# Optimization experiments

Measured on AMD Instinct MI355X. Metric: run time of the kernel, lower is better.

## Reference

```python
import jax, jax.numpy as jnp
import numpy as np
from jax import lax

EPS = 1e-12  # F.normalize eps


def setup_inputs() -> dict:
    key = jax.random.key(0)
    k1, k2, k3, k4 = jax.random.split(key, 4)
    B, C, H, W = 4, 192, 256, 256
    h = 4
    x = jax.random.normal(k1, (B, C, H, W), dtype=jnp.float32)
    qkv_w = jax.random.normal(k2, (3 * C, C), dtype=jnp.float32) * (1.0 / np.sqrt(C))
    dw_w = jax.random.normal(k3, (3 * C, 1, 3, 3), dtype=jnp.float32) * (1.0 / 3.0)
    temp = jnp.ones((h, 1, 1), dtype=jnp.float32)
    proj_w = jax.random.normal(k4, (C, C), dtype=jnp.float32) * (1.0 / np.sqrt(C))
    return {"x": x, "qkv_w": qkv_w, "dw_w": dw_w, "temp": temp, "proj_w": proj_w}


def _l2norm_lastdim(t):
    # F.normalize(t, dim=-1): divide by max(||t||_2, eps)
    n = jnp.sqrt(jnp.sum(t * t, axis=-1, keepdims=True))
    return t / jnp.maximum(n, EPS)


def reference(x, qkv_w, dw_w, temp, proj_w):
    B, C, H, W = x.shape
    h = temp.shape[0]
    D = C // h
    # 1x1 conv (qkv): [B,C,H,W] x [3C,C] -> [B,3C,H,W]
    qkv = jnp.einsum('bchw,oc->bohw', x, qkv_w)
    # depthwise 3x3 conv, padding=1, groups=3C
    qkv = lax.conv_general_dilated(
        qkv, dw_w, window_strides=(1, 1), padding='SAME',
        feature_group_count=3 * C,
        dimension_numbers=('NCHW', 'OIHW', 'NCHW'))
    q, k, v = jnp.split(qkv, 3, axis=1)
    # [B, h, D, HW]
    q = q.reshape(B, h, D, H * W)
    k = k.reshape(B, h, D, H * W)
    v = v.reshape(B, h, D, H * W)
    q = _l2norm_lastdim(q)
    k = _l2norm_lastdim(k)
    # channel attention: [B,h,D,D]
    attn = jnp.einsum('bhdn,bhen->bhde', q, k) * temp[None]
    attn = jax.nn.softmax(attn, axis=-1)
    out = jnp.einsum('bhde,bhen->bhdn', attn, v).reshape(B, C, H, W)
    # 1x1 proj
    return jnp.einsum('bchw,oc->bohw', out, proj_w)
```

## Files before the change

kernel.cpp:

```cpp
#include <hip/hip_runtime.h>

typedef unsigned int uint;
typedef unsigned short ushort;
typedef __attribute__((ext_vector_type(8))) short bf16x8;
typedef __attribute__((ext_vector_type(4))) float f32x4;

#define HWSZ 65536
#define CIN 192
#define C3 576
#define CQK 384

typedef __attribute__((address_space(1))) const void gvoid_c;
typedef __attribute__((address_space(3))) void lvoid;

__device__ __forceinline__ void async16(void* l, const void* g) {
  __builtin_amdgcn_global_load_lds((gvoid_c*)g, (lvoid*)l, 16, 0, 0);
}

__device__ __forceinline__ ushort f2bf(float f) {
  uint u = __float_as_uint(f);
  return (ushort)((u + 0x7fffu + ((u >> 16) & 1u)) >> 16);
}
__device__ __forceinline__ float bflo(uint u) { return __uint_as_float(u << 16); }
__device__ __forceinline__ float bfhi(uint u) { return __uint_as_float(u & 0xffff0000u); }

__global__ __launch_bounds__(256) void k0_transpose(const float* __restrict__ x,
                                                    ushort* __restrict__ xT) {
  __shared__ ushort lds_t[192 * 66];
  int id = blockIdx.x;
  int n0 = (id & 1023) << 6;
  int b = id >> 10;
  int tid = threadIdx.x;
  int nl = tid & 63;
  int cq = tid >> 6;
  const float* xb = x + (long)b * CIN * HWSZ + n0;
#pragma unroll 4
  for (int j = 0; j < 48; ++j) {
    int c = cq + 4 * j;
    lds_t[c * 66 + nl] = f2bf(xb[(long)c * HWSZ + nl]);
  }
  __syncthreads();
  ushort* ob = xT + (long)b * HWSZ * CIN + (long)n0 * CIN;
  int l = tid & 63, w = tid >> 6;
#pragma unroll
  for (int jj = 0; jj < 6; ++jj) {
    int n = w * 16 + (l & 15);
    int m = jj * 4 + (l >> 4);
    int cb = m * 8;
    ushort v[8];
#pragma unroll
    for (int k = 0; k < 8; ++k) v[k] = lds_t[(cb + k) * 66 + n];
    uint4 pk;
    pk.x = (uint)v[0] | ((uint)v[1] << 16);
    pk.y = (uint)v[2] | ((uint)v[3] << 16);
    pk.z = (uint)v[4] | ((uint)v[5] << 16);
    pk.w = (uint)v[6] | ((uint)v[7] << 16);
    *(uint4*)(ob + (long)n * CIN + cb) = pk;
  }
}

__global__ __launch_bounds__(256) void k0_cvtw(const float* __restrict__ w,
                                               ushort* __restrict__ wb, int nelem) {
  int i = (blockIdx.x * 256 + threadIdx.x) * 4;
  if (i + 3 < nelem) {
    float4 f = *(const float4*)(w + i);
    ushort4 o;
    o.x = f2bf(f.x); o.y = f2bf(f.y); o.z = f2bf(f.z); o.w = f2bf(f.w);
    *(ushort4*)(wb + i) = o;
  }
}

template <typename TOut>
__global__ __launch_bounds__(512, 6) void gemm_nt(const ushort* __restrict__ A, long a_bstride,
                                                  const ushort* __restrict__ B, long b_bstride,
                                                  TOut* __restrict__ D, long d_bstride,
                                                  int mtiles) {
  __shared__ ushort lds[23040];
  int idx = blockIdx.x;
  int ntile = idx & 511;
  int bm = idx >> 9;
  int mtile = bm % mtiles;
  int b = bm / mtiles;
  int tid = threadIdx.x;
  int lane = tid & 63;
  int wv = tid >> 6;
  int wm = wv >> 1, wn = wv & 1;
  int lanelo = lane & 15, laneq = lane >> 4;

  const ushort* Ab = A + a_bstride * b + (long)mtile * 192 * 192;
  const ushort* Bb = B + b_bstride * b + (long)ntile * 128 * 192;

  f32x4 acc[3][4] = {};

  for (int kit = 0; kit < 3; ++kit) {
#pragma unroll
    for (int i = 0; i < 6; ++i) {
      int wbase = i * 512 + wv * 64;
      if (wbase < 2880) {
        int c = wbase + lane;
        bool isA = c < 1728;
        int local = isA ? c : c - 1728;
        int row = local / 9;
        int sub = local % 9;
        if (sub < 8) {
          const ushort* g = (isA ? Ab : Bb) + row * 192 + kit * 64 + sub * 8;
          async16((char*)lds + wbase * 16, g);
        }
      }
    }
    __syncthreads();
#pragma unroll
    for (int ks = 0; ks < 2; ++ks) {
      bf16x8 af[3], bf[4];
#pragma unroll
      for (int mt = 0; mt < 3; ++mt) {
        int m = wm * 48 + mt * 16 + lanelo;
        af[mt] = *(const bf16x8*)((const char*)lds + m * 144 + ks * 64 + laneq * 16);
      }
#pragma unroll
      for (int nt = 0; nt < 4; ++nt) {
        int n = wn * 64 + nt * 16 + lanelo;
        bf[nt] = *(const bf16x8*)((const char*)lds + 27648 + n * 144 + ks * 64 + laneq * 16);
      }
#pragma unroll
      for (int mt = 0; mt < 3; ++mt)
#pragma unroll
        for (int nt = 0; nt < 4; ++nt)
          acc[mt][nt] = __builtin_amdgcn_mfma_f32_16x16x32_bf16(af[mt], bf[nt], acc[mt][nt], 0, 0, 0);
    }
    __syncthreads();
  }

  TOut* Db = D + d_bstride * b;
  int colb = ntile * 128 + wn * 64 + lanelo;
#pragma unroll
  for (int mt = 0; mt < 3; ++mt)
#pragma unroll
    for (int nt = 0; nt < 4; ++nt)
#pragma unroll
      for (int r = 0; r < 4; ++r) {
        long row = (long)(mtile * 192 + wm * 48 + mt * 16 + laneq * 4 + r);
        float v = acc[mt][nt][r];
        if constexpr (sizeof(TOut) == 2)
          Db[row * HWSZ + colb + nt * 16] = f2bf(v);
        else
          Db[row * HWSZ + colb + nt * 16] = v;
      }
}

template <typename TOut>
__global__ __launch_bounds__(512, 4) void gemm_nn(const ushort* __restrict__ A, long a_bstride,
                                                  const ushort* __restrict__ B, long b_bstride,
                                                  TOut* __restrict__ D, long d_bstride,
                                                  int mtiles) {
  __shared__ ushort lds[18432];
  int idx = blockIdx.x;
  int ntile = idx & 1023;
  int bm = idx >> 10;
  int mtile = bm % mtiles;
  int b = bm / mtiles;
  int tid = threadIdx.x;
  int lane = tid & 63;
  int wv = tid >> 6;
  int wm = wv >> 1, wn = wv & 1;
  int lanelo = lane & 15, laneq = lane >> 4;

  const ushort* Ab = A + a_bstride * b + (long)mtile * 192 * 192;
  const ushort* Bb = B + b_bstride * b + (long)ntile * 64;

  int cs = tid >> 3, chk = tid & 7;
  ushort* lb = lds + 13824;

  f32x4 acc[3][2] = {};

  for (int kit = 0; kit < 3; ++kit) {
    uint4 bv = *(const uint4*)(Bb + (long)(kit * 64 + cs) * HWSZ + chk * 8);
#pragma unroll
    for (int i = 0; i < 4; ++i) {
      int wbase = i * 512 + wv * 64;
      if (wbase < 1728) {
        int cc = wbase + lane;
        int row = cc / 9, sub = cc % 9;
        if (sub < 8) {
          const ushort* g = Ab + row * 192 + kit * 64 + sub * 8;
          async16((char*)lds + wbase * 16, g);
        }
      }
    }
    union { uint4 q; ushort u[8]; } pk;
    pk.q = bv;
    int colbase = (((cs >> 3) ^ chk) << 3) | (cs & 7);
#pragma unroll
    for (int j = 0; j < 8; ++j)
      lb[(chk * 8 + j) * 72 + colbase] = pk.u[j];
    __syncthreads();
#pragma unroll
    for (int ks = 0; ks < 2; ++ks) {
      bf16x8 af[3], bf[2];
#pragma unroll
      for (int mt = 0; mt < 3; ++mt) {
        int m = wm * 48 + mt * 16 + lanelo;
        af[mt] = *(const bf16x8*)((const char*)lds + m * 144 + ks * 64 + laneq * 16);
      }
#pragma unroll
      for (int nt = 0; nt < 2; ++nt) {
        int n = wn * 32 + nt * 16 + lanelo;
        int cb = ks * 4 + laneq;
        bf[nt] = *(const bf16x8*)((const char*)lds + 27648 + n * 144 +
                                  ((cb ^ ((n >> 3) & 7)) << 4));
      }
#pragma unroll
      for (int mt = 0; mt < 3; ++mt)
#pragma unroll
        for (int nt = 0; nt < 2; ++nt)
          acc[mt][nt] = __builtin_amdgcn_mfma_f32_16x16x32_bf16(af[mt], bf[nt], acc[mt][nt], 0, 0, 0);
    }
    __syncthreads();
  }

  TOut* Db = D + d_bstride * b;
  int colb = ntile * 64 + wn * 32 + lanelo;
#pragma unroll
  for (int mt = 0; mt < 3; ++mt)
#pragma unroll
    for (int nt = 0; nt < 2; ++nt)
#pragma unroll
      for (int r = 0; r < 4; ++r) {
        long row = (long)(mtile * 192 + wm * 48 + mt * 16 + laneq * 4 + r);
        float v = acc[mt][nt][r];
        if constexpr (sizeof(TOut) == 2)
          Db[row * HWSZ + colb + nt * 16] = f2bf(v);
        else
          Db[row * HWSZ + colb + nt * 16] = v;
      }
}

__global__ __launch_bounds__(256) void k2_qk(const ushort* __restrict__ qkv,
                                             ushort* __restrict__ qkdw,
                                             float* __restrict__ sqp,
                                             const float* __restrict__ dww) {
  __shared__ uint row_lds[34 * 132];
  __shared__ float red[4];
  int id = blockIdx.x;
  int yt = id & 7;
  int bc = id >> 3;
  int c = bc % CQK;
  int b = bc / CQK;
  int y0 = yt * 32;
  int tid = threadIdx.x;
  const uint* src = (const uint*)qkv + ((long)(b * C3 + c) * HWSZ >> 1);
  for (int i = tid; i < 4488; i += 256) {
    int r = i / 132, wx = i % 132;
    int gy = y0 - 1 + r;
    uint v = 0;
    if (gy >= 0 && gy < 256 && wx >= 1 && wx <= 128) v = src[gy * 128 + wx - 1];
    row_lds[i] = v;
  }
  float w9[9];
#pragma unroll
  for (int j = 0; j < 9; ++j) w9[j] = dww[c * 9 + j];
  __syncthreads();
  int row = tid >> 3;
  int xp0 = (tid & 7) * 16;
  float ss = 0.f;
  uint* dst = (uint*)qkdw + ((long)(b * CQK + c) * HWSZ >> 1) + (y0 + row) * 128 + xp0;
#pragma unroll
  for (int ch = 0; ch < 4; ++ch) {
    float o0[4] = {0.f, 0.f, 0.f, 0.f}, o1[4] = {0.f, 0.f, 0.f, 0.f};
#pragma unroll
    for (int dy = 0; dy < 3; ++dy) {
      const uint* L = &row_lds[(row + dy) * 132 + xp0 + ch * 4];
      uint4 q4 = *(const uint4*)L;
      uint2 q2 = *(const uint2*)(L + 4);
      uint u[6] = {q4.x, q4.y, q4.z, q4.w, q2.x, q2.y};
      float wa = w9[dy * 3 + 0], wb_ = w9[dy * 3 + 1], wc = w9[dy * 3 + 2];
#pragma unroll
      for (int j = 0; j < 4; ++j) {
        float f0 = bfhi(u[j]), f1 = bflo(u[j + 1]), f2 = bfhi(u[j + 1]), f3 = bflo(u[j + 2]);
        o0[j] += wa * f0 + wb_ * f1 + wc * f2;
        o1[j] += wa * f1 + wb_ * f2 + wc * f3;
      }
    }
    uint4 pk;
    pk.x = (uint)f2bf(o0[0]) | ((uint)f2bf(o1[0]) << 16);
    pk.y = (uint)f2bf(o0[1]) | ((uint)f2bf(o1[1]) << 16);
    pk.z = (uint)f2bf(o0[2]) | ((uint)f2bf(o1[2]) << 16);
    pk.w = (uint)f2bf(o0[3]) | ((uint)f2bf(o1[3]) << 16);
#pragma unroll
    for (int j = 0; j < 4; ++j) ss += o0[j] * o0[j] + o1[j] * o1[j];
    *(uint4*)(dst + ch * 4) = pk;
  }
#pragma unroll
  for (int off = 32; off; off >>= 1) ss += __shfl_down(ss, off);
  if ((tid & 63) == 0) red[tid >> 6] = ss;
  __syncthreads();
  if (tid == 0) sqp[(long)(b * CQK + c) * 8 + yt] = red[0] + red[1] + red[2] + red[3];
}

__global__ __launch_bounds__(256) void k2_vc(const ushort* __restrict__ qkv,
                                             ushort* __restrict__ vdw,
                                             const float* __restrict__ dww) {
  __shared__ uint row_lds[34 * 132];
  int id = blockIdx.x;
  int yt = id & 7;
  int bc = id >> 3;
  int c = bc % 192;
  int b = bc / 192;
  int y0 = yt * 32;
  int tid = threadIdx.x;
  const uint* src = (const uint*)qkv + ((long)(b * C3 + CQK + c) * HWSZ >> 1);
  for (int i = tid; i < 4488; i += 256) {
    int r = i / 132, wx = i % 132;
    int gy = y0 - 1 + r;
    uint v = 0;
    if (gy >= 0 && gy < 256 && wx >= 1 && wx <= 128) v = src[gy * 128 + wx - 1];
    row_lds[i] = v;
  }
  float w9[9];
#pragma unroll
  for (int j = 0; j < 9; ++j) w9[j] = dww[(CQK + c) * 9 + j];
  __syncthreads();
  int row = tid >> 3;
  int xp0 = (tid & 7) * 16;
  uint* dst = (uint*)vdw + ((long)(b * 192 + c) * HWSZ >> 1) + (y0 + row) * 128 + xp0;
#pragma unroll
  for (int ch = 0; ch < 4; ++ch) {
    float o0[4] = {0.f, 0.f, 0.f, 0.f}, o1[4] = {0.f, 0.f, 0.f, 0.f};
#pragma unroll
    for (int dy = 0; dy < 3; ++dy) {
      const uint* L = &row_lds[(row + dy) * 132 + xp0 + ch * 4];
      uint4 q4 = *(const uint4*)L;
      uint2 q2 = *(const uint2*)(L + 4);
      uint u[6] = {q4.x, q4.y, q4.z, q4.w, q2.x, q2.y};
      float wa = w9[dy * 3 + 0], wb_ = w9[dy * 3 + 1], wc = w9[dy * 3 + 2];
#pragma unroll
      for (int j = 0; j < 4; ++j) {
        float f0 = bfhi(u[j]), f1 = bflo(u[j + 1]), f2 = bfhi(u[j + 1]), f3 = bflo(u[j + 2]);
        o0[j] += wa * f0 + wb_ * f1 + wc * f2;
        o1[j] += wa * f1 + wb_ * f2 + wc * f3;
      }
    }
    uint4 pk;
    pk.x = (uint)f2bf(o0[0]) | ((uint)f2bf(o1[0]) << 16);
    pk.y = (uint)f2bf(o0[1]) | ((uint)f2bf(o1[1]) << 16);
    pk.z = (uint)f2bf(o0[2]) | ((uint)f2bf(o1[2]) << 16);
    pk.w = (uint)f2bf(o0[3]) | ((uint)f2bf(o1[3]) << 16);
    *(uint4*)(dst + ch * 4) = pk;
  }
}

__global__ __launch_bounds__(256, 4) void k3_attn(const ushort* __restrict__ qkdw,
                                                  float* __restrict__ rawp) {
  __shared__ ushort qk_lds[96 * 136];
  int id = blockIdx.x;
  int chunk = id & 31;
  int bh = id >> 5;
  int b = bh >> 2, h = bh & 3;
  int tid = threadIdx.x;
  int lane = tid & 63, wv = tid >> 6;
  int lanelo = lane & 15, laneq = lane >> 4;
  f32x4 acc[3][3] = {};
  long kbase0 = (long)chunk * 2048;
  for (int it = 0; it < 16; ++it) {
    long kb = kbase0 + it * 128;
#pragma unroll
    for (int i = 0; i < 7; ++i) {
      int wbase = i * 256 + wv * 64;
      if (wbase < 1632) {
        int cc = wbase + lane;
        if (cc < 1632) {
          int row = cc / 17, sub = cc % 17;
          if (sub < 16) {
            int chn = (row < 48) ? (h * 48 + row) : (192 + h * 48 + row - 48);
            const ushort* g = qkdw + (long)(b * CQK + chn) * HWSZ + kb + sub * 8;
            async16((char*)qk_lds + wbase * 16, g);
          }
        }
      }
    }
    __syncthreads();
    bf16x8 af[3], bf[3];
#pragma unroll
    for (int mt = 0; mt < 3; ++mt)
      af[mt] = *(const bf16x8*)((const char*)qk_lds + (mt * 16 + lanelo) * 272 + wv * 64 + laneq * 16);
#pragma unroll
    for (int et = 0; et < 3; ++et)
      bf[et] = *(const bf16x8*)((const char*)qk_lds + (48 + et * 16 + lanelo) * 272 + wv * 64 + laneq * 16);
#pragma unroll
    for (int mt = 0; mt < 3; ++mt)
#pragma unroll
      for (int et = 0; et < 3; ++et)
        acc[mt][et] = __builtin_amdgcn_mfma_f32_16x16x32_bf16(af[mt], bf[et], acc[mt][et], 0, 0, 0);
    __syncthreads();
  }
  float* rb = rawp + ((long)bh * 32 + chunk) * 2304;
#pragma unroll
  for (int mt = 0; mt < 3; ++mt)
#pragma unroll
    for (int et = 0; et < 3; ++et)
#pragma unroll
      for (int r = 0; r < 4; ++r) {
        int d = mt * 16 + laneq * 4 + r;
        int e = et * 16 + lanelo;
        rb[d * 48 + e] = acc[mt][et][r];
      }
}

__global__ __launch_bounds__(256) void k3_soft(const float* __restrict__ rawp,
                                               const float* __restrict__ sqp,
                                               const float* __restrict__ temp,
                                               const float* __restrict__ projw,
                                               ushort* __restrict__ M) {
  __shared__ float attn[48 * 48];
  __shared__ float iq[48], ik[48];
  int bh = blockIdx.x;
  int b = bh >> 2, h = bh & 3;
  int tid = threadIdx.x;
  if (tid < 48) {
    const float* p = sqp + (long)(b * CQK + h * 48 + tid) * 8;
    float s = 0.f;
#pragma unroll
    for (int k = 0; k < 8; ++k) s += p[k];
    iq[tid] = 1.f / fmaxf(sqrtf(s), 1e-12f);
  } else if (tid < 96) {
    int e = tid - 48;
    const float* p = sqp + (long)(b * CQK + 192 + h * 48 + e) * 8;
    float s = 0.f;
#pragma unroll
    for (int k = 0; k < 8; ++k) s += p[k];
    ik[e] = 1.f / fmaxf(sqrtf(s), 1e-12f);
  }
  __syncthreads();
  float t = temp[h];
  for (int i = tid; i < 2304; i += 256) {
    float s = 0.f;
    const float* rp = rawp + (long)bh * 32 * 2304 + i;
#pragma unroll 8
    for (int ch = 0; ch < 32; ++ch) s += rp[ch * 2304];
    int d = i / 48, e = i % 48;
    attn[i] = s * iq[d] * ik[e] * t;
  }
  __syncthreads();
  if (tid < 48) {
    float mx = -1e30f;
    for (int e = 0; e < 48; ++e) mx = fmaxf(mx, attn[tid * 48 + e]);
    float s = 0.f;
    for (int e = 0; e < 48; ++e) {
      float v = expf(attn[tid * 48 + e] - mx);
      attn[tid * 48 + e] = v;
      s += v;
    }
    float inv = 1.f / s;
    for (int e = 0; e < 48; ++e) attn[tid * 48 + e] *= inv;
  }
  __syncthreads();
  ushort* Mb = M + (long)b * 192 * 192;
  for (int i = tid; i < 192 * 48; i += 256) {
    int cp = i / 48, e = i % 48;
    const float* pw = projw + (long)cp * 192 + h * 48;
    float s = 0.f;
#pragma unroll 4
    for (int d = 0; d < 48; ++d) s += pw[d] * attn[d * 48 + e];
    Mb[(long)cp * 192 + h * 48 + e] = f2bf(s);
  }
}

extern "C" void kernel_launch(void* const* d_in, const int* in_sizes, int n_in,
                              void* d_out, int out_size, void* d_ws, size_t ws_size,
                              hipStream_t stream) {
  const float* x = (const float*)d_in[0];
  const float* qkv_w = (const float*)d_in[1];
  const float* dw_w = (const float*)d_in[2];
  const float* temp = (const float*)d_in[3];
  const float* proj_w = (const float*)d_in[4];

  char* ws = (char*)d_ws;
  ushort* xT = (ushort*)(ws);
  ushort* QKV = (ushort*)(ws + 100663296L);
  ushort* qkdw = (ushort*)(ws + 402653184L);
  ushort* wbf = (ushort*)(ws + 603979776L);
  ushort* Mbf = (ushort*)(ws + 604200960L);
  float* sqp = (float*)(ws + 604495872L);
  float* rawp = (float*)(ws + 604545024L);

  k0_transpose<<<4096, 256, 0, stream>>>(x, xT);
  k0_cvtw<<<108, 256, 0, stream>>>(qkv_w, wbf, 110592);
  gemm_nt<ushort><<<6144, 512, 0, stream>>>(wbf, 0L, xT, (long)HWSZ * CIN, QKV, (long)C3 * HWSZ, 3);
  k2_qk<<<12288, 256, 0, stream>>>(QKV, qkdw, sqp, dw_w);
  k2_vc<<<6144, 256, 0, stream>>>(QKV, xT, dw_w);
  k3_attn<<<512, 256, 0, stream>>>(qkdw, rawp);
  k3_soft<<<16, 256, 0, stream>>>(rawp, sqp, temp, proj_w, Mbf);
  gemm_nn<float><<<4096, 512, 0, stream>>>(Mbf, (long)192 * 192, xT, (long)192 * HWSZ,
                                           (float*)d_out, (long)CIN * HWSZ, 1);
}
```

Measured before the change: 1.040 ms.

## Fuse fp32-to-bf16 input conversion into NN GEMM and drop transpose kernel

Removes the separate transpose/convert kernel and has the QKV 1x1-conv GEMM read fp32 x directly in its native channel-major layout, converting to bf16 while staging into LDS. The NT GEMM is deleted and the templated NN GEMM, now with a higher occupancy hint, handles both projections. This saves a full read and write pass over x. In exchange the GEMM reads twice as many bytes for B, and the 64-wide N tiles mean the fp32 input is loaded three times, once per M tile.

```diff
diff --git a/kernel.cpp b/kernel.cpp
--- a/kernel.cpp
+++ b/kernel.cpp
@@ -23,41 +23,6 @@
 }
 __device__ __forceinline__ float bflo(uint u) { return __uint_as_float(u << 16); }
 __device__ __forceinline__ float bfhi(uint u) { return __uint_as_float(u & 0xffff0000u); }
-
-__global__ __launch_bounds__(256) void k0_transpose(const float* __restrict__ x,
-                                                    ushort* __restrict__ xT) {
-  __shared__ ushort lds_t[192 * 66];
-  int id = blockIdx.x;
-  int n0 = (id & 1023) << 6;
-  int b = id >> 10;
-  int tid = threadIdx.x;
-  int nl = tid & 63;
-  int cq = tid >> 6;
-  const float* xb = x + (long)b * CIN * HWSZ + n0;
-#pragma unroll 4
-  for (int j = 0; j < 48; ++j) {
-    int c = cq + 4 * j;
-    lds_t[c * 66 + nl] = f2bf(xb[(long)c * HWSZ + nl]);
-  }
-  __syncthreads();
-  ushort* ob = xT + (long)b * HWSZ * CIN + (long)n0 * CIN;
-  int l = tid & 63, w = tid >> 6;
-#pragma unroll
-  for (int jj = 0; jj < 6; ++jj) {
-    int n = w * 16 + (l & 15);
-    int m = jj * 4 + (l >> 4);
-    int cb = m * 8;
-    ushort v[8];
-#pragma unroll
-    for (int k = 0; k < 8; ++k) v[k] = lds_t[(cb + k) * 66 + n];
-    uint4 pk;
-    pk.x = (uint)v[0] | ((uint)v[1] << 16);
-    pk.y = (uint)v[2] | ((uint)v[3] << 16);
-    pk.z = (uint)v[4] | ((uint)v[5] << 16);
-    pk.w = (uint)v[6] | ((uint)v[7] << 16);
-    *(uint4*)(ob + (long)n * CIN + cb) = pk;
-  }
-}
 
 __global__ __launch_bounds__(256) void k0_cvtw(const float* __restrict__ w,
                                                ushort* __restrict__ wb, int nelem) {
@@ -70,87 +35,9 @@
   }
 }
 
-template <typename TOut>
-__global__ __launch_bounds__(512, 6) void gemm_nt(const ushort* __restrict__ A, long a_bstride,
-                                                  const ushort* __restrict__ B, long b_bstride,
-                                                  TOut* __restrict__ D, long d_bstride,
-                                                  int mtiles) {
-  __shared__ ushort lds[23040];
-  int idx = blockIdx.x;
-  int ntile = idx & 511;
-  int bm = idx >> 9;
-  int mtile = bm % mtiles;
-  int b = bm / mtiles;
-  int tid = threadIdx.x;
-  int lane = tid & 63;
-  int wv = tid >> 6;
-  int wm = wv >> 1, wn = wv & 1;
-  int lanelo = lane & 15, laneq = lane >> 4;
-
-  const ushort* Ab = A + a_bstride * b + (long)mtile * 192 * 192;
-  const ushort* Bb = B + b_bstride * b + (long)ntile * 128 * 192;
-
-  f32x4 acc[3][4] = {};
-
-  for (int kit = 0; kit < 3; ++kit) {
-#pragma unroll
-    for (int i = 0; i < 6; ++i) {
-      int wbase = i * 512 + wv * 64;
-      if (wbase < 2880) {
-        int c = wbase + lane;
-        bool isA = c < 1728;
-        int local = isA ? c : c - 1728;
-        int row = local / 9;
-        int sub = local % 9;
-        if (sub < 8) {
-          const ushort* g = (isA ? Ab : Bb) + row * 192 + kit * 64 + sub * 8;
-          async16((char*)lds + wbase * 16, g);
-        }
-      }
-    }
-    __syncthreads();
-#pragma unroll
-    for (int ks = 0; ks < 2; ++ks) {
-      bf16x8 af[3], bf[4];
-#pragma unroll
-      for (int mt = 0; mt < 3; ++mt) {
-        int m = wm * 48 + mt * 16 + lanelo;
-        af[mt] = *(const bf16x8*)((const char*)lds + m * 144 + ks * 64 + laneq * 16);
-      }
-#pragma unroll
-      for (int nt = 0; nt < 4; ++nt) {
-        int n = wn * 64 + nt * 16 + lanelo;
-        bf[nt] = *(const bf16x8*)((const char*)lds + 27648 + n * 144 + ks * 64 + laneq * 16);
-      }
-#pragma unroll
-      for (int mt = 0; mt < 3; ++mt)
-#pragma unroll
-        for (int nt = 0; nt < 4; ++nt)
-          acc[mt][nt] = __builtin_amdgcn_mfma_f32_16x16x32_bf16(af[mt], bf[nt], acc[mt][nt], 0, 0, 0);
-    }
-    __syncthreads();
-  }
-
-  TOut* Db = D + d_bstride * b;
-  int colb = ntile * 128 + wn * 64 + lanelo;
-#pragma unroll
-  for (int mt = 0; mt < 3; ++mt)
-#pragma unroll
-    for (int nt = 0; nt < 4; ++nt)
-#pragma unroll
-      for (int r = 0; r < 4; ++r) {
-        long row = (long)(mtile * 192 + wm * 48 + mt * 16 + laneq * 4 + r);
-        float v = acc[mt][nt][r];
-        if constexpr (sizeof(TOut) == 2)
-          Db[row * HWSZ + colb + nt * 16] = f2bf(v);
-        else
-          Db[row * HWSZ + colb + nt * 16] = v;
-      }
-}
-
-template <typename TOut>
-__global__ __launch_bounds__(512, 4) void gemm_nn(const ushort* __restrict__ A, long a_bstride,
-                                                  const ushort* __restrict__ B, long b_bstride,
+template <typename TIn, typename TOut>
+__global__ __launch_bounds__(512, 6) void gemm_nn(const ushort* __restrict__ A, long a_bstride,
+                                                  const TIn* __restrict__ B, long b_bstride,
                                                   TOut* __restrict__ D, long d_bstride,
                                                   int mtiles) {
   __shared__ ushort lds[18432];
@@ -166,7 +53,7 @@
   int lanelo = lane & 15, laneq = lane >> 4;
 
   const ushort* Ab = A + a_bstride * b + (long)mtile * 192 * 192;
-  const ushort* Bb = B + b_bstride * b + (long)ntile * 64;
+  const TIn* Bb = B + b_bstride * b + (long)ntile * 64;
 
   int cs = tid >> 3, chk = tid & 7;
   ushort* lb = lds + 13824;
@@ -174,7 +61,19 @@
   f32x4 acc[3][2] = {};
 
   for (int kit = 0; kit < 3; ++kit) {
-    uint4 bv = *(const uint4*)(Bb + (long)(kit * 64 + cs) * HWSZ + chk * 8);
+    const TIn* bsrc = Bb + (long)(kit * 64 + cs) * HWSZ + chk * 8;
+    ushort u8[8];
+    if constexpr (sizeof(TIn) == 4) {
+      float4 f0 = *(const float4*)bsrc;
+      float4 f1 = *(const float4*)(bsrc + 4);
+      u8[0] = f2bf(f0.x); u8[1] = f2bf(f0.y); u8[2] = f2bf(f0.z); u8[3] = f2bf(f0.w);
+      u8[4] = f2bf(f1.x); u8[5] = f2bf(f1.y); u8[6] = f2bf(f1.z); u8[7] = f2bf(f1.w);
+    } else {
+      union { uint4 q; ushort u[8]; } pk;
+      pk.q = *(const uint4*)bsrc;
+#pragma unroll
+      for (int j = 0; j < 8; ++j) u8[j] = pk.u[j];
+    }
 #pragma unroll
     for (int i = 0; i < 4; ++i) {
       int wbase = i * 512 + wv * 64;
@@ -187,12 +86,10 @@
         }
       }
     }
-    union { uint4 q; ushort u[8]; } pk;
-    pk.q = bv;
     int colbase = (((cs >> 3) ^ chk) << 3) | (cs & 7);
 #pragma unroll
     for (int j = 0; j < 8; ++j)
-      lb[(chk * 8 + j) * 72 + colbase] = pk.u[j];
+      lb[(chk * 8 + j) * 72 + colbase] = u8[j];
     __syncthreads();
 #pragma unroll
     for (int ks = 0; ks < 2; ++ks) {
@@ -475,7 +372,7 @@
   const float* proj_w = (const float*)d_in[4];
 
   char* ws = (char*)d_ws;
-  ushort* xT = (ushort*)(ws);
+  ushort* vdw = (ushort*)(ws);
   ushort* QKV = (ushort*)(ws + 100663296L);
   ushort* qkdw = (ushort*)(ws + 402653184L);
   ushort* wbf = (ushort*)(ws + 603979776L);
@@ -483,13 +380,13 @@
   float* sqp = (float*)(ws + 604495872L);
   float* rawp = (float*)(ws + 604545024L);
 
-  k0_transpose<<<4096, 256, 0, stream>>>(x, xT);
   k0_cvtw<<<108, 256, 0, stream>>>(qkv_w, wbf, 110592);
-  gemm_nt<ushort><<<6144, 512, 0, stream>>>(wbf, 0L, xT, (long)HWSZ * CIN, QKV, (long)C3 * HWSZ, 3);
+  gemm_nn<float, ushort><<<12288, 512, 0, stream>>>(wbf, 0L, x, (long)CIN * HWSZ,
+                                                    QKV, (long)C3 * HWSZ, 3);
   k2_qk<<<12288, 256, 0, stream>>>(QKV, qkdw, sqp, dw_w);
-  k2_vc<<<6144, 256, 0, stream>>>(QKV, xT, dw_w);
+  k2_vc<<<6144, 256, 0, stream>>>(QKV, vdw, dw_w);
   k3_attn<<<512, 256, 0, stream>>>(qkdw, rawp);
   k3_soft<<<16, 256, 0, stream>>>(rawp, sqp, temp, proj_w, Mbf);
-  gemm_nn<float><<<4096, 512, 0, stream>>>(Mbf, (long)192 * 192, xT, (long)192 * HWSZ,
-                                           (float*)d_out, (long)CIN * HWSZ, 1);
-}
+  gemm_nn<ushort, float><<<4096, 512, 0, stream>>>(Mbf, (long)192 * 192, vdw, (long)192 * HWSZ,
+                                                   (float*)d_out, (long)CIN * HWSZ, 1);
+}
```

New measurement: 833.2 us. 19.9% less time.
